# Performance work log

Hardware: AMD Instinct MI355X
Metric: run time of the kernel (lower is better)

Reference implementation:

```python
import jax, jax.numpy as jnp
import numpy as np

FEATURE_DIM = 1024
MAX_DEPTH = 32
HID = 128
N = 32768


def setup_inputs() -> dict:
    key = jax.random.key(0)
    ks = jax.random.split(key, 16)
    d = FEATURE_DIM
    s = 0.02
    return {
        "features": jax.random.normal(ks[0], (N, d), jnp.float32),
        "depths": jax.random.randint(ks[1], (N,), 0, MAX_DEPTH),
        "pos_emb": jax.random.normal(ks[2], (MAX_DEPTH, d), jnp.float32) * s,
        "aW1": jax.random.normal(ks[3], (HID, 2 * d), jnp.float32) * s,
        "ab1": jnp.zeros((HID,), jnp.float32),
        "aW2": jax.random.normal(ks[4], (1, HID), jnp.float32) * s,
        "ab2": jnp.zeros((1,), jnp.float32),
        "uW1": jax.random.normal(ks[5], (d, 2 * d), jnp.float32) * s,
        "ub1": jnp.zeros((d,), jnp.float32),
        "uW2": jax.random.normal(ks[6], (d, d), jnp.float32) * s,
        "ub2": jnp.zeros((d,), jnp.float32),
        "gW": jax.random.normal(ks[7], (d, 2 * d), jnp.float32) * s,
        "gb": jnp.zeros((d,), jnp.float32),
    }


def reference(features, depths, pos_emb, aW1, ab1, aW2, ab2,
              uW1, ub1, uW2, ub2, gW, gb):
    # add position embeddings (depths clamped to [0, MAX_DEPTH-1])
    dep = jnp.clip(depths, 0, MAX_DEPTH - 1)
    f = features + pos_emb[dep]                       # [N, d]
    target = f[0:1]                                    # [1, d]
    path = f[1:]                                       # [N-1, d]

    # attention MLP over all path states at once (vectorizes the torch loop)
    tb = jnp.broadcast_to(target, path.shape)          # [N-1, d]
    comb = jnp.concatenate([tb, path], axis=1)         # [N-1, 2d]
    h = jax.nn.relu(comb @ aW1.T + ab1)                # [N-1, 128]
    attn = jax.nn.sigmoid(h @ aW2.T + ab2)             # [N-1, 1]

    s = attn.sum()
    attn = jnp.where(s > 0, attn / s, attn)

    agg = (path * attn).sum(axis=0, keepdims=True)     # [1, d]
    c2 = jnp.concatenate([target, agg], axis=1)        # [1, 2d]
    gate = jax.nn.sigmoid(c2 @ gW.T + gb)
    upd = jax.nn.relu(c2 @ uW1.T + ub1) @ uW2.T + ub2
    updated_target = target + gate * upd
    return jnp.concatenate([updated_target, path], axis=0)
```

## Files before the change

### kernel.cpp

```cpp
#include <hip/hip_runtime.h>

#define DNUM 1024
#define HIDN 128
#define NTOT 32768
#define MR 32
#define NBLK 1024

#define T_OFF 0
#define P0_OFF 1024
#define S_OFF 1152
#define AGG_OFF 1216
#define GATE_OFF 2240
#define U1_OFF 3264
#define W2_FOFF 4288
#define AGGP_OFF (W2_FOFF + 65536)
#define SP_OFF (AGGP_OFF + NBLK * DNUM)
#define WS_NEED ((size_t)(SP_OFF + NBLK) * 4)

typedef __attribute__((ext_vector_type(8))) short short8;
typedef __attribute__((ext_vector_type(4))) float f32x4;

__device__ __forceinline__ unsigned short f2bf(float x) {
  unsigned int u = __builtin_bit_cast(unsigned int, x);
  u = u + 0x7fffu + ((u >> 16) & 1u);
  return (unsigned short)(u >> 16);
}
__device__ __forceinline__ float bf2f(unsigned int bits16) {
  unsigned int u = bits16 << 16;
  return __builtin_bit_cast(float, u);
}

__global__ __launch_bounds__(256) void ka(const float* __restrict__ features,
                                          const int* __restrict__ depths,
                                          const float* __restrict__ pos_emb,
                                          float* __restrict__ ws) {
  int t = threadIdx.x;
  int dep = depths[0];
  dep = dep < 0 ? 0 : (dep > 31 ? 31 : dep);
  float4 fv = *(const float4*)(features + t * 4);
  float4 pe = *(const float4*)(pos_emb + dep * DNUM + t * 4);
  float4 r;
  r.x = fv.x + pe.x; r.y = fv.y + pe.y; r.z = fv.z + pe.z; r.w = fv.w + pe.w;
  *(float4*)(ws + T_OFF + t * 4) = r;
  float4 z = make_float4(0.f, 0.f, 0.f, 0.f);
  *(float4*)(ws + AGG_OFF + t * 4) = z;
  if (t < 64) ws[S_OFF + t] = 0.f;
}

__global__ __launch_bounds__(256) void kaw(const float* __restrict__ aW1,
                                           const float* __restrict__ ab1,
                                           float* __restrict__ ws,
                                           unsigned short* __restrict__ w2) {
  int t = threadIdx.x, bid = blockIdx.x;
  if (bid == 0) {
    __shared__ float ph[256];
    int j = t >> 1, h = t & 1;
    const float* wrow = aW1 + (size_t)j * (2 * DNUM) + h * 512;
    const float* tr = ws + T_OFF + h * 512;
    float p = 0.f;
    for (int k = 0; k < 512; k += 4) {
      float4 wv = *(const float4*)(wrow + k);
      float4 tv = *(const float4*)(tr + k);
      p += wv.x * tv.x + wv.y * tv.y + wv.z * tv.z + wv.w * tv.w;
    }
    ph[t] = p;
    __syncthreads();
    if (t < HIDN) ws[P0_OFF + t] = ab1[t] + ph[t * 2] + ph[t * 2 + 1];
    return;
  }
  int idx = ((bid - 1) * 256 + t) * 4;
  int j = idx >> 10, k = idx & 1023;
  float4 v = *(const float4*)(aW1 + (size_t)j * 2048 + 1024 + k);
  uint2 pk;
  pk.x = (unsigned int)f2bf(v.x) | ((unsigned int)f2bf(v.y) << 16);
  pk.y = (unsigned int)f2bf(v.z) | ((unsigned int)f2bf(v.w) << 16);
  *(uint2*)(w2 + idx) = pk;
}

__global__ __launch_bounds__(512, 4) void kbig(
    const float* __restrict__ features, const int* __restrict__ depths,
    const float* __restrict__ pos_emb, const float* __restrict__ p0,
    const float* __restrict__ aW2, const float* __restrict__ ab2,
    const unsigned short* __restrict__ w2, float* __restrict__ out,
    float* __restrict__ agg, float* __restrict__ sacc,
    float* __restrict__ aggp, float* __restrict__ sp) {
  __shared__ __align__(16) unsigned char ldsA[MR * 2048];
  __shared__ int depsL[MR];
  __shared__ float part[160];
  __shared__ float comb[1024];
  const int t = threadIdx.x;
  const int bid = blockIdx.x;
  const int lane = t & 63;
  const int w = t >> 6;
  const int llo = lane & 15;
  const int lhi = lane >> 4;
  const int tc = t & 255;
  const int th = t >> 8;
  const int col = tc * 4;

  if (t < MR) {
    int fr = 1 + bid * MR + t;
    int dp = (fr < NTOT) ? depths[fr] : 0;
    dp = dp < 0 ? 0 : (dp > 31 ? 31 : dp);
    depsL[t] = dp;
  }
  __syncthreads();

  for (int ii = 0; ii < 16; ++ii) {
    int i = ii * 2 + th;
    int fr = 1 + bid * MR + i;
    float4 f = make_float4(0.f, 0.f, 0.f, 0.f);
    if (fr < NTOT) {
      float4 fv = *(const float4*)(features + (size_t)fr * DNUM + col);
      float4 pe = *(const float4*)(pos_emb + depsL[i] * DNUM + col);
      f.x = fv.x + pe.x; f.y = fv.y + pe.y; f.z = fv.z + pe.z; f.w = fv.w + pe.w;
      f32x4 fe = {f.x, f.y, f.z, f.w};
      __builtin_nontemporal_store(fe, (f32x4*)(out + (size_t)fr * DNUM + col));
    }
    uint2 pk;
    pk.x = (unsigned int)f2bf(f.x) | ((unsigned int)f2bf(f.y) << 16);
    pk.y = (unsigned int)f2bf(f.z) | ((unsigned int)f2bf(f.w) << 16);
    int off = (i * 2048 + tc * 8) ^ ((i & 7) << 4);
    *(uint2*)(ldsA + off) = pk;
  }
  __syncthreads();

  const int wm = w >> 2, wn = w & 3;
  f32x4 acc[2];
  acc[0] = (f32x4){0.f, 0.f, 0.f, 0.f};
  acc[1] = (f32x4){0.f, 0.f, 0.f, 0.f};
  const int arow = wm * 16 + llo;
  const int abase = arow * 2048;
  const int aswz = (arow & 7) << 4;
  const unsigned short* bpA = w2 + (size_t)(wn * 32 + llo) * DNUM + lhi * 8;
  const unsigned short* bpB = bpA + 16 * DNUM;

#pragma unroll 4
  for (int kc = 0; kc < 32; ++kc) {
    int kbase = kc * 32;
    short8 av = *(short8*)(ldsA + ((abase + (kbase + lhi * 8) * 2) ^ aswz));
    short8 bv0 = *(const short8*)(bpA + kbase);
    short8 bv1 = *(const short8*)(bpB + kbase);
    acc[0] = __builtin_amdgcn_mfma_f32_16x16x32_bf16(av, bv0, acc[0], 0, 0, 0);
    acc[1] = __builtin_amdgcn_mfma_f32_16x16x32_bf16(av, bv1, acc[1], 0, 0, 0);
  }

  float p0v[2], wv[2];
#pragma unroll
  for (int n = 0; n < 2; ++n) {
    int j = wn * 32 + n * 16 + llo;
    p0v[n] = p0[j];
    wv[n] = aW2[j];
  }
#pragma unroll
  for (int e = 0; e < 4; ++e) {
    float s = 0.f;
#pragma unroll
    for (int n = 0; n < 2; ++n) {
      float h = acc[n][e] + p0v[n];
      h = fmaxf(h, 0.f);
      s += h * wv[n];
    }
    s += __shfl_xor(s, 1);
    s += __shfl_xor(s, 2);
    s += __shfl_xor(s, 4);
    s += __shfl_xor(s, 8);
    if (llo == 0) part[wn * 32 + wm * 16 + lhi * 4 + e] = s;
  }
  __syncthreads();

  if (t < MR) {
    float pre = part[t] + part[32 + t] + part[64 + t] + part[96 + t] + ab2[0];
    int fr = 1 + bid * MR + t;
    float raw = 0.f;
    if (fr < NTOT) raw = 1.f / (1.f + __expf(-pre));
    part[128 + t] = raw;
  }
  __syncthreads();

  float a0 = 0.f, a1 = 0.f, a2 = 0.f, a3 = 0.f;
  for (int lr = th * 16; lr < th * 16 + 16; ++lr) {
    float r = part[128 + lr];
    int off = (lr * 2048 + tc * 8) ^ ((lr & 7) << 4);
    uint2 pk = *(uint2*)(ldsA + off);
    a0 += r * bf2f(pk.x & 0xffffu);
    a1 += r * bf2f(pk.x >> 16);
    a2 += r * bf2f(pk.y & 0xffffu);
    a3 += r * bf2f(pk.y >> 16);
  }
  if (th == 1) {
    comb[tc * 4 + 0] = a0; comb[tc * 4 + 1] = a1;
    comb[tc * 4 + 2] = a2; comb[tc * 4 + 3] = a3;
  }
  __syncthreads();
  if (th == 0) {
    float c0 = a0 + comb[tc * 4 + 0];
    float c1 = a1 + comb[tc * 4 + 1];
    float c2v = a2 + comb[tc * 4 + 2];
    float c3 = a3 + comb[tc * 4 + 3];
    if (aggp) {
      f32x4 v = {c0, c1, c2v, c3};
      *(f32x4*)(aggp + (size_t)bid * DNUM + col) = v;
    } else {
      atomicAdd(agg + col + 0, c0);
      atomicAdd(agg + col + 1, c1);
      atomicAdd(agg + col + 2, c2v);
      atomicAdd(agg + col + 3, c3);
    }
  }
  if (t == 0) {
    float s = 0.f;
    for (int lr = 0; lr < MR; ++lr) s += part[128 + lr];
    if (sp) sp[bid] = s;
    else atomicAdd(sacc + (bid & 63), s);
  }
}

__global__ __launch_bounds__(256) void kred(const float* __restrict__ aggp,
                                            const float* __restrict__ sp,
                                            float* __restrict__ ws) {
  int t = threadIdx.x, bid = blockIdx.x;
  if (bid < 256) {
    int w = t >> 6, lane = t & 63;
    int colIdx = bid * 4 + w;
    float s = 0.f;
#pragma unroll 4
    for (int k = 0; k < 16; ++k) {
      int r = lane + k * 64;
      s += aggp[(size_t)r * DNUM + colIdx];
    }
    s += __shfl_xor(s, 1);
    s += __shfl_xor(s, 2);
    s += __shfl_xor(s, 4);
    s += __shfl_xor(s, 8);
    s += __shfl_xor(s, 16);
    s += __shfl_xor(s, 32);
    if (lane == 0) ws[AGG_OFF + colIdx] = s;
  } else {
    __shared__ float red[256];
    float s = sp[t] + sp[t + 256] + sp[t + 512] + sp[t + 768];
    red[t] = s;
    __syncthreads();
    if (t < 64) {
      float v = red[t] + red[t + 64] + red[t + 128] + red[t + 192];
      v += __shfl_xor(v, 1);
      v += __shfl_xor(v, 2);
      v += __shfl_xor(v, 4);
      v += __shfl_xor(v, 8);
      v += __shfl_xor(v, 16);
      v += __shfl_xor(v, 32);
      if (t == 0) ws[S_OFF] = v;
    }
  }
}

__global__ __launch_bounds__(256) void kc1(const float* __restrict__ gW,
                                           const float* __restrict__ gb,
                                           const float* __restrict__ uW1,
                                           const float* __restrict__ ub1,
                                           float* __restrict__ ws) {
  __shared__ float c2[2048];
  __shared__ float sinv_sh;
  int t = threadIdx.x, bid = blockIdx.x;
  if (t == 0) {
    float s = 0.f;
    for (int i = 0; i < 64; ++i) s += ws[S_OFF + i];
    sinv_sh = (s > 0.f) ? 1.f / s : 1.f;
  }
  __syncthreads();
  float sinv = sinv_sh;
  for (int i = t; i < 2048; i += 256)
    c2[i] = (i < 1024) ? ws[T_OFF + i] : ws[AGG_OFF + i - 1024] * sinv;
  __syncthreads();
  int w = t >> 6, lane = t & 63;
  int isGate = bid < 256;
  int o = (isGate ? bid : bid - 256) * 4 + w;
  const float* W = isGate ? gW : uW1;
  float p = 0.f;
  for (int i = lane; i < 2048; i += 64) p += W[(size_t)o * 2048 + i] * c2[i];
  p += __shfl_xor(p, 1);
  p += __shfl_xor(p, 2);
  p += __shfl_xor(p, 4);
  p += __shfl_xor(p, 8);
  p += __shfl_xor(p, 16);
  p += __shfl_xor(p, 32);
  if (lane == 0) {
    float v = p + (isGate ? gb[o] : ub1[o]);
    v = isGate ? (1.f / (1.f + expf(-v))) : fmaxf(v, 0.f);
    ws[(isGate ? GATE_OFF : U1_OFF) + o] = v;
  }
}

__global__ __launch_bounds__(256) void kc2(const float* __restrict__ uW2,
                                           const float* __restrict__ ub2,
                                           const float* __restrict__ ws,
                                           float* __restrict__ out) {
  __shared__ float u1[1024];
  int t = threadIdx.x, bid = blockIdx.x;
  for (int i = t; i < 1024; i += 256) u1[i] = ws[U1_OFF + i];
  __syncthreads();
  int w = t >> 6, lane = t & 63;
  int o = bid * 4 + w;
  float p = 0.f;
  for (int i = lane; i < 1024; i += 64) p += uW2[(size_t)o * 1024 + i] * u1[i];
  p += __shfl_xor(p, 1);
  p += __shfl_xor(p, 2);
  p += __shfl_xor(p, 4);
  p += __shfl_xor(p, 8);
  p += __shfl_xor(p, 16);
  p += __shfl_xor(p, 32);
  if (lane == 0) {
    float upd = p + ub2[o];
    out[o] = ws[T_OFF + o] + ws[GATE_OFF + o] * upd;
  }
}

extern "C" void kernel_launch(void* const* d_in, const int* in_sizes, int n_in,
                              void* d_out, int out_size, void* d_ws, size_t ws_size,
                              hipStream_t stream) {
  const float* features = (const float*)d_in[0];
  const int* depths = (const int*)d_in[1];
  const float* pos_emb = (const float*)d_in[2];
  const float* aW1 = (const float*)d_in[3];
  const float* ab1 = (const float*)d_in[4];
  const float* aW2 = (const float*)d_in[5];
  const float* ab2 = (const float*)d_in[6];
  const float* uW1 = (const float*)d_in[7];
  const float* ub1 = (const float*)d_in[8];
  const float* uW2 = (const float*)d_in[9];
  const float* ub2 = (const float*)d_in[10];
  const float* gW = (const float*)d_in[11];
  const float* gb = (const float*)d_in[12];
  float* out = (float*)d_out;
  float* ws = (float*)d_ws;
  unsigned short* w2 = (unsigned short*)(ws + W2_FOFF);
  bool useP = ws_size >= WS_NEED;
  float* aggp = useP ? (ws + AGGP_OFF) : nullptr;
  float* sp = useP ? (ws + SP_OFF) : nullptr;

  hipLaunchKernelGGL(ka, dim3(1), dim3(256), 0, stream, features, depths, pos_emb, ws);
  hipLaunchKernelGGL(kaw, dim3(129), dim3(256), 0, stream, aW1, ab1, ws, w2);
  hipLaunchKernelGGL(kbig, dim3(NBLK), dim3(512), 0, stream, features, depths, pos_emb,
                     ws + P0_OFF, aW2, ab2, w2, out, ws + AGG_OFF, ws + S_OFF, aggp, sp);
  if (useP)
    hipLaunchKernelGGL(kred, dim3(257), dim3(256), 0, stream, aggp, sp, ws);
  hipLaunchKernelGGL(kc1, dim3(512), dim3(256), 0, stream, gW, gb, uW1, ub1, ws);
  hipLaunchKernelGGL(kc2, dim3(256), dim3(256), 0, stream, uW2, ub2, ws, out);
}
```

Before: 160.3 us.

## Split fused stream+GEMM kernel into separate streaming and GEMM passes, merge init kernels

Folds the target-row setup kernel into the weight-conversion kernel, saving one launch and one global round trip for the target row. The big fused kernel is split in two. A simple streaming kernel now adds position embeddings and writes the output. A separate GEMM kernel then reads the combined rows back from the output buffer for the attention MLP. This removes per-block depth staging and simplifies the GEMM kernel. The cost is a second full pass over the output tensor, which depends on cache residency, and the aggregate buffer is no longer zeroed at init.

New measurement: 179.9 us. 12.3% more time.

```diff
diff --git a/kernel.cpp b/kernel.cpp
--- a/kernel.cpp
+++ b/kernel.cpp
@@ -30,33 +30,30 @@
   return __builtin_bit_cast(float, u);
 }
 
-__global__ __launch_bounds__(256) void ka(const float* __restrict__ features,
-                                          const int* __restrict__ depths,
-                                          const float* __restrict__ pos_emb,
-                                          float* __restrict__ ws) {
-  int t = threadIdx.x;
-  int dep = depths[0];
-  dep = dep < 0 ? 0 : (dep > 31 ? 31 : dep);
-  float4 fv = *(const float4*)(features + t * 4);
-  float4 pe = *(const float4*)(pos_emb + dep * DNUM + t * 4);
-  float4 r;
-  r.x = fv.x + pe.x; r.y = fv.y + pe.y; r.z = fv.z + pe.z; r.w = fv.w + pe.w;
-  *(float4*)(ws + T_OFF + t * 4) = r;
-  float4 z = make_float4(0.f, 0.f, 0.f, 0.f);
-  *(float4*)(ws + AGG_OFF + t * 4) = z;
-  if (t < 64) ws[S_OFF + t] = 0.f;
-}
-
-__global__ __launch_bounds__(256) void kaw(const float* __restrict__ aW1,
-                                           const float* __restrict__ ab1,
-                                           float* __restrict__ ws,
-                                           unsigned short* __restrict__ w2) {
+__global__ __launch_bounds__(256) void kinit(const float* __restrict__ features,
+                                             const int* __restrict__ depths,
+                                             const float* __restrict__ pos_emb,
+                                             const float* __restrict__ aW1,
+                                             const float* __restrict__ ab1,
+                                             float* __restrict__ ws,
+                                             unsigned short* __restrict__ w2) {
   int t = threadIdx.x, bid = blockIdx.x;
   if (bid == 0) {
+    __shared__ float tgt[1024];
     __shared__ float ph[256];
+    int dep = depths[0];
+    dep = dep < 0 ? 0 : (dep > 31 ? 31 : dep);
+    float4 fv = *(const float4*)(features + t * 4);
+    float4 pe = *(const float4*)(pos_emb + dep * DNUM + t * 4);
+    float4 r;
+    r.x = fv.x + pe.x; r.y = fv.y + pe.y; r.z = fv.z + pe.z; r.w = fv.w + pe.w;
+    *(float4*)(ws + T_OFF + t * 4) = r;
+    *(float4*)(tgt + t * 4) = r;
+    if (t < 64) ws[S_OFF + t] = 0.f;
+    __syncthreads();
     int j = t >> 1, h = t & 1;
     const float* wrow = aW1 + (size_t)j * (2 * DNUM) + h * 512;
-    const float* tr = ws + T_OFF + h * 512;
+    const float* tr = tgt + h * 512;
     float p = 0.f;
     for (int k = 0; k < 512; k += 4) {
       float4 wv = *(const float4*)(wrow + k);
@@ -77,15 +74,35 @@
   *(uint2*)(w2 + idx) = pk;
 }
 
-__global__ __launch_bounds__(512, 4) void kbig(
-    const float* __restrict__ features, const int* __restrict__ depths,
-    const float* __restrict__ pos_emb, const float* __restrict__ p0,
+__global__ __launch_bounds__(256) void kstream(const float* __restrict__ features,
+                                               const int* __restrict__ depths,
+                                               const float* __restrict__ pos_emb,
+                                               float* __restrict__ out) {
+  const int t = threadIdx.x;
+  const int bid = blockIdx.x;
+  const int col = t * 4;
+#pragma unroll
+  for (int rr = 0; rr < 4; ++rr) {
+    int fr = 1 + bid * 4 + rr;
+    if (fr < NTOT) {
+      int dp = depths[fr];
+      dp = dp < 0 ? 0 : (dp > 31 ? 31 : dp);
+      float4 fv = *(const float4*)(features + (size_t)fr * DNUM + col);
+      float4 pe = *(const float4*)(pos_emb + (size_t)dp * DNUM + col);
+      float4 f;
+      f.x = fv.x + pe.x; f.y = fv.y + pe.y; f.z = fv.z + pe.z; f.w = fv.w + pe.w;
+      *(float4*)(out + (size_t)fr * DNUM + col) = f;
+    }
+  }
+}
+
+__global__ __launch_bounds__(512, 4) void kgemm(
+    const float* __restrict__ fsrc, const float* __restrict__ p0,
     const float* __restrict__ aW2, const float* __restrict__ ab2,
-    const unsigned short* __restrict__ w2, float* __restrict__ out,
+    const unsigned short* __restrict__ w2,
     float* __restrict__ agg, float* __restrict__ sacc,
     float* __restrict__ aggp, float* __restrict__ sp) {
   __shared__ __align__(16) unsigned char ldsA[MR * 2048];
-  __shared__ int depsL[MR];
   __shared__ float part[160];
   __shared__ float comb[1024];
   const int t = threadIdx.x;
@@ -98,25 +115,12 @@
   const int th = t >> 8;
   const int col = tc * 4;
 
-  if (t < MR) {
-    int fr = 1 + bid * MR + t;
-    int dp = (fr < NTOT) ? depths[fr] : 0;
-    dp = dp < 0 ? 0 : (dp > 31 ? 31 : dp);
-    depsL[t] = dp;
-  }
-  __syncthreads();
-
+#pragma unroll
   for (int ii = 0; ii < 16; ++ii) {
     int i = ii * 2 + th;
     int fr = 1 + bid * MR + i;
-    float4 f = make_float4(0.f, 0.f, 0.f, 0.f);
-    if (fr < NTOT) {
-      float4 fv = *(const float4*)(features + (size_t)fr * DNUM + col);
-      float4 pe = *(const float4*)(pos_emb + depsL[i] * DNUM + col);
-      f.x = fv.x + pe.x; f.y = fv.y + pe.y; f.z = fv.z + pe.z; f.w = fv.w + pe.w;
-      f32x4 fe = {f.x, f.y, f.z, f.w};
-      __builtin_nontemporal_store(fe, (f32x4*)(out + (size_t)fr * DNUM + col));
-    }
+    float4 f = (fr < NTOT) ? *(const float4*)(fsrc + (size_t)fr * DNUM + col)
+                           : make_float4(0.f, 0.f, 0.f, 0.f);
     uint2 pk;
     pk.x = (unsigned int)f2bf(f.x) | ((unsigned int)f2bf(f.y) << 16);
     pk.y = (unsigned int)f2bf(f.z) | ((unsigned int)f2bf(f.w) << 16);
@@ -338,10 +342,12 @@
   float* aggp = useP ? (ws + AGGP_OFF) : nullptr;
   float* sp = useP ? (ws + SP_OFF) : nullptr;
 
-  hipLaunchKernelGGL(ka, dim3(1), dim3(256), 0, stream, features, depths, pos_emb, ws);
-  hipLaunchKernelGGL(kaw, dim3(129), dim3(256), 0, stream, aW1, ab1, ws, w2);
-  hipLaunchKernelGGL(kbig, dim3(NBLK), dim3(512), 0, stream, features, depths, pos_emb,
-                     ws + P0_OFF, aW2, ab2, w2, out, ws + AGG_OFF, ws + S_OFF, aggp, sp);
+  hipLaunchKernelGGL(kinit, dim3(129), dim3(256), 0, stream,
+                     features, depths, pos_emb, aW1, ab1, ws, w2);
+  hipLaunchKernelGGL(kstream, dim3(8192), dim3(256), 0, stream,
+                     features, depths, pos_emb, out);
+  hipLaunchKernelGGL(kgemm, dim3(NBLK), dim3(512), 0, stream,
+                     out, ws + P0_OFF, aW2, ab2, w2, ws + AGG_OFF, ws + S_OFF, aggp, sp);
   if (useP)
     hipLaunchKernelGGL(kred, dim3(257), dim3(256), 0, stream, aggp, sp, ws);
   hipLaunchKernelGGL(kc1, dim3(512), dim3(256), 0, stream, gW, gb, uW1, ub1, ws);
```
